# Performance work log

Hardware: AMD Instinct MI355X
Metric: run time of the kernel (lower is better)

## Reference

```python
import jax, jax.numpy as jnp
import numpy as np

BINS = 5
POINTS = 2
EPS_DIV = 1e-6
GN_GROUPS = 32
GN_EPS = 1e-5


def bilinear_sum(img, ys, xs):
    """Sum of bilinear samples with zero padding outside the image.
    img: (B, C, H, W); ys, xs: (B, K, H, W) absolute sample coords.
    Returns (B, C, H, W) = sum over K of bilinear(img, ys_k, xs_k)."""
    B, C, H, W = img.shape
    K = ys.shape[1]
    y0 = jnp.floor(ys)
    x0 = jnp.floor(xs)
    imgf = img.reshape(B, C, H * W)
    acc = jnp.zeros((B, C, K, H, W), img.dtype)
    for dy, dx in ((0, 0), (0, 1), (1, 0), (1, 1)):
        yi = y0 + dy
        xi = x0 + dx
        w = (1.0 - jnp.abs(ys - yi)) * (1.0 - jnp.abs(xs - xi))
        valid = (yi >= 0) & (yi <= H - 1) & (xi >= 0) & (xi <= W - 1)
        yc = jnp.clip(yi, 0, H - 1).astype(jnp.int32)
        xc = jnp.clip(xi, 0, W - 1).astype(jnp.int32)
        idx = (yc * W + xc).reshape(B, 1, K * H * W)
        g = jnp.take_along_axis(imgf, idx, axis=2).reshape(B, C, K, H, W)
        acc = acc + (w * valid.astype(img.dtype))[:, None] * g
    return acc.sum(axis=2)


def setup_inputs():
    key = jax.random.key(0)
    ks = jax.random.split(key, 6)
    B, C, H, W = 2, 256, 100, 152
    P, K = POINTS, BINS
    x = jax.random.normal(ks[0], (B, C, H, W), jnp.float32)
    offsets = jax.random.normal(ks[1], (B, P * K * 2, H, W), jnp.float32) * 2.0
    ef_w = jax.random.normal(ks[2], (P * C, C), jnp.float32) * 0.02
    ef_b = jnp.zeros((P * C,), jnp.float32)
    hm1_w = jax.random.normal(ks[3], (P, C, C), jnp.float32) * 0.02
    hm1_b = jnp.zeros((P, C), jnp.float32)
    hm2_w = jax.random.normal(ks[4], (P, C), jnp.float32) * 0.02
    hm2_b = jnp.zeros((P,), jnp.float32)
    merge_w = jax.random.normal(ks[5], (C, P * C), jnp.float32) * 0.02
    merge_b = jnp.zeros((C,), jnp.float32)
    gn_g = jnp.ones((C,), jnp.float32)
    gn_b = jnp.zeros((C,), jnp.float32)
    return {"x": x, "offsets": offsets, "ef_w": ef_w, "ef_b": ef_b,
            "hm1_w": hm1_w, "hm1_b": hm1_b, "hm2_w": hm2_w, "hm2_b": hm2_b,
            "merge_w": merge_w, "merge_b": merge_b, "gn_g": gn_g, "gn_b": gn_b}


def reference(x, offsets, ef_w, ef_b, hm1_w, hm1_b, hm2_w, hm2_b, merge_w, merge_b, gn_g, gn_b):
    B, C, H, W = x.shape
    P, K = POINTS, BINS
    # expand_feat: 1x1 conv C -> P*C
    ef = jnp.einsum('bchw,dc->bdhw', x, ef_w) + ef_b[None, :, None, None]
    efp = ef.reshape(B, P, C, H, W)
    # heatmap: grouped 1x1 conv (per-point) -> ReLU -> grouped 1x1 conv -> exp
    h = jax.nn.relu(jnp.einsum('bpchw,pdc->bpdhw', efp, hm1_w) + hm1_b[None, :, :, None, None])
    heat = jnp.exp(jnp.einsum('bpdhw,pd->bphw', h, hm2_w) + hm2_b[None, :, None, None])  # (B,P,H,W)
    # offsets: (B, P, K, 2, H, W) with channel layout [y, x] per bin.
    # base_offset cancels the [1,bins] kernel grid, so the deform conv with
    # all-ones weights is simply: sum over bins of bilinear samples at
    # (h + off_y, w + off_x).
    off = offsets.reshape(B, P, K, 2, H, W)
    hg = jnp.arange(H, dtype=x.dtype)[None, None, None, :, None]
    wg = jnp.arange(W, dtype=x.dtype)[None, None, None, None, :]
    ys = hg + off[:, :, :, 0]  # (B,P,K,H,W)
    xs = wg + off[:, :, :, 1]
    outs = []
    for p in range(P):
        # sample feat*heat (C channels) and heat (1 channel) together
        img = jnp.concatenate([efp[:, p] * heat[:, p][:, None], heat[:, p][:, None]], axis=1)
        s = bilinear_sum(img, ys[:, p], xs[:, p])  # (B, C+1, H, W)
        outs.append(s[:, :C] / (s[:, C:] + EPS_DIV))
    outs = jnp.concatenate(outs, axis=1)  # (B, P*C, H, W)
    merged = jnp.einsum('bchw,dc->bdhw', outs, merge_w) + merge_b[None, :, None, None]
    # GroupNorm(32, C) + ReLU
    g = merged.reshape(B, GN_GROUPS, C // GN_GROUPS, H, W)
    mu = g.mean(axis=(2, 3, 4), keepdims=True)
    var = g.var(axis=(2, 3, 4), keepdims=True)
    gn = ((g - mu) / jnp.sqrt(var + GN_EPS)).reshape(B, C, H, W)
    gn = gn * gn_g[None, :, None, None] + gn_b[None, :, None, None]
    return jax.nn.relu(gn)
```

## Files before the change

kernel.cpp:

```cpp
#include <hip/hip_runtime.h>

#define BINS 5
#define PTS  2
constexpr int Bx = 2, Cc = 256, Hh = 100, Ww = 152;
constexpr int HW = Hh * Ww;
constexpr int NTILE = 238;
constexpr float EPS_DIV = 1e-6f;
constexpr float GN_EPS  = 1e-5f;

typedef __attribute__((ext_vector_type(8))) _Float16 hfrag;
typedef __attribute__((ext_vector_type(2))) _Float16 h2;
typedef __attribute__((ext_vector_type(4))) float f32x4;

__device__ __forceinline__ ushort f2h(float f) {
    return __builtin_bit_cast(ushort, (_Float16)f);
}
__device__ __forceinline__ float hlo(unsigned u) {
    return (float)__builtin_bit_cast(_Float16, (ushort)(u & 0xffffu));
}
__device__ __forceinline__ float hhi(unsigned u) {
    return (float)__builtin_bit_cast(_Float16, (ushort)(u >> 16));
}

__global__ __launch_bounds__(256)
void k_wconv(const float* __restrict__ efw, const float* __restrict__ w1,
             const float* __restrict__ mw, ushort* __restrict__ wb)
{
    int gid = blockIdx.x * 256 + threadIdx.x;
    int e = gid * 4;
    int arr = e >> 17, off = e & 131071;
    const float* src = arr == 0 ? efw : (arr == 1 ? w1 : mw);
    float4 v = *(const float4*)(src + off);
    ushort4 o = { f2h(v.x), f2h(v.y), f2h(v.z), f2h(v.w) };
    *(ushort4*)(wb + e) = o;
}

__global__ __launch_bounds__(256)
void k_xt(const float* __restrict__ x, ushort* __restrict__ xbt)
{
    __shared__ float tile[32][33];
    const int t = threadIdx.x;
    const int hw0 = blockIdx.x * 32;
    const int c0 = blockIdx.y * 32;
    const int b = blockIdx.z;
    const float* xb = x + ((size_t)b * Cc + c0) * HW + hw0;
    const int tx = t & 31, ty = t >> 5;
    #pragma unroll
    for (int r = 0; r < 4; r++) {
        int c = ty + r * 8;
        tile[c][tx] = xb[(size_t)c * HW + tx];
    }
    __syncthreads();
    const int hwl = t >> 3, c4 = (t & 7) * 4;
    ushort4 o = { f2h(tile[c4 + 0][hwl]), f2h(tile[c4 + 1][hwl]),
                  f2h(tile[c4 + 2][hwl]), f2h(tile[c4 + 3][hwl]) };
    *(ushort4*)&xbt[((size_t)b * HW + hw0 + hwl) * Cc + c0 + c4] = o;
}

__global__ __launch_bounds__(256)
void k_ef(const ushort* __restrict__ xbt, const ushort* __restrict__ wbe,
          const float* __restrict__ efb, ushort* __restrict__ efp)
{
    __shared__ ushort As[128 * 72];
    __shared__ ushort Bs[64 * 72];
    const int t = threadIdx.x;
    const int wv = t >> 6, ln = t & 63;
    const int quad = ln >> 4, l16 = ln & 15;
    const int pix0 = blockIdx.x * 64;
    const int n0 = blockIdx.y * 128;
    const int b = blockIdx.z;
    const ushort* xb = xbt + (size_t)b * HW * Cc;

    f32x4 acc[2][4];
    #pragma unroll
    for (int i = 0; i < 2; i++)
        #pragma unroll
        for (int j = 0; j < 4; j++) acc[i][j] = (f32x4){0.f, 0.f, 0.f, 0.f};

    const int arow = t >> 3, acol = (t & 7) * 8;
    const int srow = t >> 3, scol = (t & 7) * 8;

    for (int k0 = 0; k0 < 256; k0 += 64) {
        #pragma unroll
        for (int r = 0; r < 4; r++) {
            int row = arow + r * 32;
            *(uint4*)&As[row * 72 + acol] =
                *(const uint4*)&wbe[(size_t)(n0 + row) * 256 + k0 + acol];
        }
        #pragma unroll
        for (int r = 0; r < 2; r++) {
            int row = srow + r * 32;
            int pq = pix0 + row; if (pq > HW - 1) pq = HW - 1;
            *(uint4*)&Bs[row * 72 + scol] =
                *(const uint4*)&xb[(size_t)pq * Cc + k0 + scol];
        }
        __syncthreads();
        #pragma unroll
        for (int kk = 0; kk < 64; kk += 32) {
            hfrag af[2], bfr[4];
            #pragma unroll
            for (int dt = 0; dt < 2; dt++)
                af[dt] = *(const hfrag*)&As[(wv * 32 + dt * 16 + l16) * 72 + kk + quad * 8];
            #pragma unroll
            for (int pt = 0; pt < 4; pt++)
                bfr[pt] = *(const hfrag*)&Bs[(pt * 16 + l16) * 72 + kk + quad * 8];
            #pragma unroll
            for (int dt = 0; dt < 2; dt++)
                #pragma unroll
                for (int pt = 0; pt < 4; pt++)
                    acc[dt][pt] = __builtin_amdgcn_mfma_f32_16x16x32_f16(
                        af[dt], bfr[pt], acc[dt][pt], 0, 0, 0);
        }
        __syncthreads();
    }

    float bias[2][4];
    #pragma unroll
    for (int dt = 0; dt < 2; dt++)
        #pragma unroll
        for (int r = 0; r < 4; r++)
            bias[dt][r] = efb[n0 + wv * 32 + dt * 16 + quad * 4 + r];
    #pragma unroll
    for (int dt = 0; dt < 2; dt++)
        #pragma unroll
        for (int pt = 0; pt < 4; pt++) {
            int pix = pt * 16 + l16;
            int ch = wv * 32 + dt * 16 + quad * 4;
            ushort4 o = { f2h(acc[dt][pt][0] + bias[dt][0]),
                          f2h(acc[dt][pt][1] + bias[dt][1]),
                          f2h(acc[dt][pt][2] + bias[dt][2]),
                          f2h(acc[dt][pt][3] + bias[dt][3]) };
            *(ushort4*)&As[pix * 136 + ch] = o;
        }
    __syncthreads();
    const int p = n0 >> 8, cbase = n0 & 255;
    ushort* outb = efp + (size_t)((b * PTS + p) * HW) * Cc;
    #pragma unroll
    for (int r = 0; r < 4; r++) {
        int pix = (t >> 4) + r * 16;
        int ch8 = (t & 15) * 8;
        if (pix0 + pix < HW)
            *(uint4*)&outb[(size_t)(pix0 + pix) * Cc + cbase + ch8] =
                *(const uint4*)&As[pix * 136 + ch8];
    }
}

__global__ __launch_bounds__(256)
void k_heat(const ushort* __restrict__ efp, const ushort* __restrict__ wb1,
            const float* __restrict__ b1, const float* __restrict__ w2,
            const float* __restrict__ b2, float* __restrict__ heat)
{
    __shared__ ushort As[256 * 72];
    __shared__ ushort Bs[64 * 72];
    __shared__ float red[4][64];
    const int t = threadIdx.x;
    const int wv = t >> 6, ln = t & 63;
    const int quad = ln >> 4, l16 = ln & 15;
    const int pix0 = blockIdx.x * 64;
    const int p = blockIdx.y;
    const int b = blockIdx.z;
    const ushort* efb_ = efp + (size_t)((b * PTS + p) * HW) * Cc;
    const ushort* w1p = wb1 + (size_t)p * Cc * Cc;

    f32x4 acc[4][4];
    #pragma unroll
    for (int i = 0; i < 4; i++)
        #pragma unroll
        for (int j = 0; j < 4; j++) acc[i][j] = (f32x4){0.f, 0.f, 0.f, 0.f};

    const int srow = t >> 3, scol = (t & 7) * 8;

    for (int k0 = 0; k0 < 256; k0 += 64) {
        #pragma unroll
        for (int r = 0; r < 8; r++) {
            int row = srow + r * 32;
            *(uint4*)&As[row * 72 + scol] =
                *(const uint4*)&w1p[(size_t)row * 256 + k0 + scol];
        }
        #pragma unroll
        for (int r = 0; r < 2; r++) {
            int row = srow + r * 32;
            int pq = pix0 + row; if (pq > HW - 1) pq = HW - 1;
            *(uint4*)&Bs[row * 72 + scol] =
                *(const uint4*)&efb_[(size_t)pq * Cc + k0 + scol];
        }
        __syncthreads();
        #pragma unroll
        for (int kk = 0; kk < 64; kk += 32) {
            hfrag af[4], bfr[4];
            #pragma unroll
            for (int dt = 0; dt < 4; dt++)
                af[dt] = *(const hfrag*)&As[(wv * 64 + dt * 16 + l16) * 72 + kk + quad * 8];
            #pragma unroll
            for (int pt = 0; pt < 4; pt++)
                bfr[pt] = *(const hfrag*)&Bs[(pt * 16 + l16) * 72 + kk + quad * 8];
            #pragma unroll
            for (int dt = 0; dt < 4; dt++)
                #pragma unroll
                for (int pt = 0; pt < 4; pt++)
                    acc[dt][pt] = __builtin_amdgcn_mfma_f32_16x16x32_f16(
                        af[dt], bfr[pt], acc[dt][pt], 0, 0, 0);
        }
        __syncthreads();
    }

    const float* b1p = b1 + p * 256;
    const float* w2p = w2 + p * 256;
    float s[4] = {0.f, 0.f, 0.f, 0.f};
    #pragma unroll
    for (int dt = 0; dt < 4; dt++) {
        int chb = wv * 64 + dt * 16 + quad * 4;
        float bb[4], ww[4];
        #pragma unroll
        for (int r = 0; r < 4; r++) { bb[r] = b1p[chb + r]; ww[r] = w2p[chb + r]; }
        #pragma unroll
        for (int pt = 0; pt < 4; pt++)
            #pragma unroll
            for (int r = 0; r < 4; r++) {
                float h = acc[dt][pt][r] + bb[r];
                h = h > 0.f ? h : 0.f;
                s[pt] += ww[r] * h;
            }
    }
    #pragma unroll
    for (int pt = 0; pt < 4; pt++) {
        s[pt] += __shfl_xor(s[pt], 16);
        s[pt] += __shfl_xor(s[pt], 32);
    }
    if (ln < 16) {
        #pragma unroll
        for (int pt = 0; pt < 4; pt++) red[wv][pt * 16 + ln] = s[pt];
    }
    __syncthreads();
    if (t < 64) {
        float v = red[0][t] + red[1][t] + red[2][t] + red[3][t] + b2[p];
        int m = pix0 + t;
        if (m < HW) heat[(size_t)(b * PTS + p) * HW + m] = expf(v);
    }
}

__global__ __launch_bounds__(256)
void k_sample(const ushort* __restrict__ efp, const float* __restrict__ heat,
              const float* __restrict__ offs, ushort* __restrict__ outs)
{
    __shared__ uint2 s_wo[32][20];
    const int t = threadIdx.x;
    const int bid = blockIdx.x;
    const int nx = (bid & 7) * 60 + (bid >> 3);
    if (nx >= 475) return;
    const int m0 = nx * 32;
    const int p = blockIdx.y;
    const int b = blockIdx.z;
    const float* heat_bp = heat + (size_t)(b * PTS + p) * HW;

    if (t < 32 * BINS) {
        int j = t / BINS, k = t % BINS;
        int hw = m0 + j;
        int hh = hw / Ww, ww = hw % Ww;
        int chy = (p * BINS + k) * 2;
        float oy = offs[((size_t)b * (PTS * BINS * 2) + chy)     * HW + hw];
        float ox = offs[((size_t)b * (PTS * BINS * 2) + chy + 1) * HW + hw];
        float ysf = (float)hh + oy;
        float xsf = (float)ww + ox;
        float y0 = floorf(ysf), x0 = floorf(xsf);
        #pragma unroll
        for (int dy = 0; dy < 2; dy++)
            #pragma unroll
            for (int dx = 0; dx < 2; dx++) {
                float yi = y0 + dy, xi = x0 + dx;
                float wgt = (1.f - fabsf(ysf - yi)) * (1.f - fabsf(xsf - xi));
                bool valid = (yi >= 0.f) && (yi <= (float)(Hh - 1)) &&
                             (xi >= 0.f) && (xi <= (float)(Ww - 1));
                int yc = (int)yi; yc = yc < 0 ? 0 : (yc > Hh - 1 ? Hh - 1 : yc);
                int xc = (int)xi; xc = xc < 0 ? 0 : (xc > Ww - 1 ? Ww - 1 : xc);
                int idx = yc * Ww + xc;
                float wh = valid ? wgt * heat_bp[idx] : 0.f;
                s_wo[j][k * 4 + dy * 2 + dx] =
                    make_uint2(__float_as_uint(wh), (unsigned)idx << 9);
            }
    }
    __syncthreads();
    if (t < 32) {
        float s = 0.f;
        #pragma unroll
        for (int u = 0; u < 20; u++) s += __uint_as_float(s_wo[t][u].x);
        float inv = 1.f / (s + EPS_DIV);
        #pragma unroll
        for (int u = 0; u < 20; u++) {
            float w = __uint_as_float(s_wo[t][u].x) * inv;
            unsigned hw16 = (unsigned)f2h(w);
            s_wo[t][u].x = hw16 | (hw16 << 16);
        }
    }
    __syncthreads();

    const int wv = t >> 6, ln = t & 63;
    const int half = ln >> 5, c8 = ln & 31;
    const char* efbase = (const char*)(efp + (size_t)((b * PTS + p) * HW) * Cc)
                         + c8 * 16;
    ushort* ob = outs + ((size_t)(b * HW + m0)) * (PTS * Cc) + p * Cc + c8 * 8;
    #pragma unroll
    for (int i = 0; i < 8; i += 2) {
        const int j = wv * 8 + i + half;
        h2 a0 = (h2){0, 0}, a1 = (h2){0, 0}, a2 = (h2){0, 0}, a3 = (h2){0, 0};
        #pragma unroll
        for (int u = 0; u < 20; u++) {
            uint2 wo = s_wo[j][u];
            uint4 v = *(const uint4*)(efbase + wo.y);
            h2 wp = __builtin_bit_cast(h2, wo.x);
            a0 += wp * __builtin_bit_cast(h2, v.x);
            a1 += wp * __builtin_bit_cast(h2, v.y);
            a2 += wp * __builtin_bit_cast(h2, v.z);
            a3 += wp * __builtin_bit_cast(h2, v.w);
        }
        uint4 o = { __builtin_bit_cast(unsigned, a0), __builtin_bit_cast(unsigned, a1),
                    __builtin_bit_cast(unsigned, a2), __builtin_bit_cast(unsigned, a3) };
        *(uint4*)(ob + (size_t)j * (PTS * Cc)) = o;
    }
}

__global__ __launch_bounds__(256)
void k_merge(const ushort* __restrict__ outs, const ushort* __restrict__ wbm,
             const float* __restrict__ mb, ushort* __restrict__ mgb,
             float* __restrict__ part2)
{
    __shared__ ushort As[64 * 72];
    __shared__ ushort Bs[64 * 72];
    const int t = threadIdx.x;
    const int wv = t >> 6, ln = t & 63;
    const int quad = ln >> 4, l16 = ln & 15;
    const int pix0 = blockIdx.x * 64;
    const int n0 = blockIdx.y * 64;
    const int b = blockIdx.z;
    const ushort* ob = outs + (size_t)b * HW * (PTS * Cc);

    f32x4 acc[4];
    #pragma unroll
    for (int j = 0; j < 4; j++) acc[j] = (f32x4){0.f, 0.f, 0.f, 0.f};

    const int srow = t >> 3, scol = (t & 7) * 8;

    for (int k0 = 0; k0 < 512; k0 += 64) {
        #pragma unroll
        for (int r = 0; r < 2; r++) {
            int row = srow + r * 32;
            *(uint4*)&As[row * 72 + scol] =
                *(const uint4*)&wbm[(size_t)(n0 + row) * 512 + k0 + scol];
        }
        #pragma unroll
        for (int r = 0; r < 2; r++) {
            int row = srow + r * 32;
            int pq = pix0 + row; if (pq > HW - 1) pq = HW - 1;
            *(uint4*)&Bs[row * 72 + scol] =
                *(const uint4*)&ob[(size_t)pq * (PTS * Cc) + k0 + scol];
        }
        __syncthreads();
        #pragma unroll
        for (int kk = 0; kk < 64; kk += 32) {
            hfrag af = *(const hfrag*)&As[(wv * 16 + l16) * 72 + kk + quad * 8];
            #pragma unroll
            for (int pt = 0; pt < 4; pt++) {
                hfrag bfr = *(const hfrag*)&Bs[(pt * 16 + l16) * 72 + kk + quad * 8];
                acc[pt] = __builtin_amdgcn_mfma_f32_16x16x32_f16(
                    af, bfr, acc[pt], 0, 0, 0);
            }
        }
        __syncthreads();
    }

    const int ch = n0 + wv * 16 + quad * 4;
    float bias[4];
    #pragma unroll
    for (int r = 0; r < 4; r++) bias[r] = mb[ch + r];

    float sacc = 0.f, qacc = 0.f;
    #pragma unroll
    for (int pt = 0; pt < 4; pt++) {
        int pix = pix0 + pt * 16 + l16;
        if (pix < HW) {
            #pragma unroll
            for (int r = 0; r < 4; r++) {
                float v = acc[pt][r] + bias[r];
                mgb[((size_t)b * Cc + ch + r) * HW + pix] = f2h(v);
                sacc += v; qacc += v * v;
            }
        }
    }
    #pragma unroll
    for (int off = 1; off <= 16; off <<= 1) {
        sacc += __shfl_xor(sacc, off);
        qacc += __shfl_xor(qacc, off);
    }
    if ((ln & 31) == 0) {
        int g = (n0 >> 3) + wv * 2 + (quad >> 1);
        size_t idx = ((size_t)(b * 32 + g) * NTILE + blockIdx.x) * 2;
        part2[idx + 0] = sacc;
        part2[idx + 1] = qacc;
    }
}

__global__ __launch_bounds__(256)
void k_gnfinal(const float* __restrict__ part2, float* __restrict__ statf)
{
    const int bg = blockIdx.x;
    const int t = threadIdx.x;
    float s = 0.f, q = 0.f;
    if (t < NTILE) {
        s = part2[((size_t)bg * NTILE + t) * 2 + 0];
        q = part2[((size_t)bg * NTILE + t) * 2 + 1];
    }
    #pragma unroll
    for (int off = 1; off <= 32; off <<= 1) {
        s += __shfl_xor(s, off);
        q += __shfl_xor(q, off);
    }
    __shared__ float rs[4], rq[4];
    int wid = t >> 6;
    if ((t & 63) == 0) { rs[wid] = s; rq[wid] = q; }
    __syncthreads();
    if (t == 0) {
        float S = rs[0] + rs[1] + rs[2] + rs[3];
        float Q = rq[0] + rq[1] + rq[2] + rq[3];
        const float n = 8.f * HW;
        float mean = S / n;
        float var  = Q / n - mean * mean;
        statf[bg * 2 + 0] = mean;
        statf[bg * 2 + 1] = rsqrtf(var + GN_EPS);
    }
}

__global__ __launch_bounds__(256)
void k_gnapply(const ushort* __restrict__ mgb, const float* __restrict__ statf,
               const float* __restrict__ gg, const float* __restrict__ gb,
               float* __restrict__ out)
{
    const int i8 = blockIdx.x * 256 + threadIdx.x;
    const int i = i8 * 8;
    const int CHW = Cc * HW;
    const int b = i / CHW;
    const int r = i - b * CHW;
    const int c = r / HW;
    const int g = c >> 3;
    float mean = statf[(b * 32 + g) * 2 + 0];
    float istd = statf[(b * 32 + g) * 2 + 1];
    float sc = istd * gg[c];
    float sh = gb[c] - mean * sc;
    uint4 v = *(const uint4*)(mgb + i);
    float4 o0, o1;
    o0.x = fmaxf(hlo(v.x) * sc + sh, 0.f);
    o0.y = fmaxf(hhi(v.x) * sc + sh, 0.f);
    o0.z = fmaxf(hlo(v.y) * sc + sh, 0.f);
    o0.w = fmaxf(hhi(v.y) * sc + sh, 0.f);
    o1.x = fmaxf(hlo(v.z) * sc + sh, 0.f);
    o1.y = fmaxf(hhi(v.z) * sc + sh, 0.f);
    o1.z = fmaxf(hlo(v.w) * sc + sh, 0.f);
    o1.w = fmaxf(hhi(v.w) * sc + sh, 0.f);
    *(float4*)(out + i)     = o0;
    *(float4*)(out + i + 4) = o1;
}

extern "C" void kernel_launch(void* const* d_in, const int* in_sizes, int n_in,
                              void* d_out, int out_size, void* d_ws, size_t ws_size,
                              hipStream_t stream)
{
    const float* x    = (const float*)d_in[0];
    const float* offs = (const float*)d_in[1];
    const float* efw  = (const float*)d_in[2];
    const float* efb  = (const float*)d_in[3];
    const float* w1   = (const float*)d_in[4];
    const float* b1   = (const float*)d_in[5];
    const float* w2   = (const float*)d_in[6];
    const float* b2   = (const float*)d_in[7];
    const float* mw   = (const float*)d_in[8];
    const float* mb   = (const float*)d_in[9];
    const float* gg   = (const float*)d_in[10];
    const float* gb   = (const float*)d_in[11];
    float* out = (float*)d_out;

    ushort* wb    = (ushort*)d_ws;
    ushort* wbe   = wb;
    ushort* wb1   = wb + 131072;
    ushort* wbm   = wb + 262144;
    ushort* efp   = wb + 393216;
    ushort* outsb = efp + (size_t)Bx * PTS * HW * Cc;
    ushort* xbt   = outsb + (size_t)Bx * HW * PTS * Cc;
    ushort* mgb   = xbt + (size_t)Bx * HW * Cc;
    float*  heat  = (float*)(mgb + (size_t)Bx * Cc * HW);
    float*  part2 = heat + (size_t)Bx * PTS * HW;
    float*  statf = part2 + (size_t)64 * NTILE * 2;

    dim3 blk(256);
    k_wconv  <<<dim3(384),              blk, 0, stream>>>(efw, w1, mw, wb);
    k_xt     <<<dim3(475, 8, Bx),       blk, 0, stream>>>(x, xbt);
    k_ef     <<<dim3(238, 4, Bx),       blk, 0, stream>>>(xbt, wbe, efb, efp);
    k_heat   <<<dim3(238, PTS, Bx),     blk, 0, stream>>>(efp, wb1, b1, w2, b2, heat);
    k_sample <<<dim3(480, PTS, Bx),     blk, 0, stream>>>(efp, heat, offs, outsb);
    k_merge  <<<dim3(NTILE, 4, Bx),     blk, 0, stream>>>(outsb, wbm, mb, mgb, part2);
    k_gnfinal<<<dim3(64),               blk, 0, stream>>>(part2, statf);
    k_gnapply<<<dim3(Bx * Cc * HW / 8 / 256), blk, 0, stream>>>(mgb, statf, gg, gb, out);
}
```

Measured before the change: 208.0 us.

## Make expand and heat GEMMs persistent with resident weights and async LDS double-buffering

The expand-feature and heatmap 1x1-conv GEMMs become persistent 512-thread blocks. Each block loads its full 128x256 weight slice into LDS once with direct global-to-LDS loads, then loops over pixel tiles using double-buffered, XOR-swizzled B tiles with vmcnt-based waits. This is meant to stop reloading weights for every tile and to hide global-load latency. Heat is split across two channel halves that write partial sums, and a new small kernel adds them with the bias and applies exp. The cost is one extra launch, much larger LDS per block, and fewer blocks (240 per kernel) to keep the GPU busy.

```diff
diff --git a/kernel.cpp b/kernel.cpp
--- a/kernel.cpp
+++ b/kernel.cpp
@@ -22,6 +22,10 @@
     return (float)__builtin_bit_cast(_Float16, (ushort)(u >> 16));
 }
 
+#define GLL16(g, l) __builtin_amdgcn_global_load_lds( \
+    (const __attribute__((address_space(1))) unsigned*)(g), \
+    (__attribute__((address_space(3))) unsigned*)(l), 16, 0, 0)
+
 __global__ __launch_bounds__(256)
 void k_wconv(const float* __restrict__ efw, const float* __restrict__ w1,
              const float* __restrict__ mw, ushort* __restrict__ wb)
@@ -57,186 +61,254 @@
     *(ushort4*)&xbt[((size_t)b * HW + hw0 + hwl) * Cc + c0 + c4] = o;
 }
 
-__global__ __launch_bounds__(256)
+__global__ __launch_bounds__(512)
 void k_ef(const ushort* __restrict__ xbt, const ushort* __restrict__ wbe,
           const float* __restrict__ efb, ushort* __restrict__ efp)
 {
-    __shared__ ushort As[128 * 72];
-    __shared__ ushort Bs[64 * 72];
-    const int t = threadIdx.x;
+    __shared__ ushort Alds[128 * 256];
+    __shared__ ushort Bl0[64 * 256];
+    __shared__ ushort Bl1[64 * 256];
+    const int t  = threadIdx.x;
     const int wv = t >> 6, ln = t & 63;
     const int quad = ln >> 4, l16 = ln & 15;
-    const int pix0 = blockIdx.x * 64;
-    const int n0 = blockIdx.y * 128;
-    const int b = blockIdx.z;
+    const int mwv = wv & 3, ngr = wv >> 2;
+    const int xr = l16 & 7;
+    const int bx = blockIdx.x;
+    const int n0 = blockIdx.y;
+    const int b  = blockIdx.z;
     const ushort* xb = xbt + (size_t)b * HW * Cc;
-
-    f32x4 acc[2][4];
-    #pragma unroll
-    for (int i = 0; i < 2; i++)
-        #pragma unroll
-        for (int j = 0; j < 4; j++) acc[i][j] = (f32x4){0.f, 0.f, 0.f, 0.f};
-
-    const int arow = t >> 3, acol = (t & 7) * 8;
-    const int srow = t >> 3, scol = (t & 7) * 8;
-
-    for (int k0 = 0; k0 < 256; k0 += 64) {
-        #pragma unroll
-        for (int r = 0; r < 4; r++) {
-            int row = arow + r * 32;
-            *(uint4*)&As[row * 72 + acol] =
-                *(const uint4*)&wbe[(size_t)(n0 + row) * 256 + k0 + acol];
-        }
-        #pragma unroll
-        for (int r = 0; r < 2; r++) {
-            int row = srow + r * 32;
-            int pq = pix0 + row; if (pq > HW - 1) pq = HW - 1;
-            *(uint4*)&Bs[row * 72 + scol] =
-                *(const uint4*)&xb[(size_t)pq * Cc + k0 + scol];
-        }
-        __syncthreads();
-        #pragma unroll
-        for (int kk = 0; kk < 64; kk += 32) {
-            hfrag af[2], bfr[4];
-            #pragma unroll
-            for (int dt = 0; dt < 2; dt++)
-                af[dt] = *(const hfrag*)&As[(wv * 32 + dt * 16 + l16) * 72 + kk + quad * 8];
-            #pragma unroll
-            for (int pt = 0; pt < 4; pt++)
-                bfr[pt] = *(const hfrag*)&Bs[(pt * 16 + l16) * 72 + kk + quad * 8];
-            #pragma unroll
-            for (int dt = 0; dt < 2; dt++)
-                #pragma unroll
-                for (int pt = 0; pt < 4; pt++)
-                    acc[dt][pt] = __builtin_amdgcn_mfma_f32_16x16x32_f16(
-                        af[dt], bfr[pt], acc[dt][pt], 0, 0, 0);
-        }
-        __syncthreads();
-    }
+    const ushort* wA = wbe + (size_t)n0 * 128 * 256;
+    const int ntl = (237 - bx) / 30 + 1;
+
+    #pragma unroll
+    for (int j = 0; j < 8; j++) {
+        int unit = j * 512 + t;
+        int row = unit >> 5, c8 = unit & 31;
+        const ushort* g = wA + row * 256 + ((c8 ^ (row & 7)) << 3);
+        ushort* l = Alds + (j * 512 + wv * 64) * 8;
+        GLL16(g, l);
+    }
+    auto stageB = [&](int tt, ushort* dst) {
+        int tp0 = tt * 64;
+        #pragma unroll
+        for (int j = 0; j < 4; j++) {
+            int unit = j * 512 + t;
+            int prow = unit >> 5, c8 = unit & 31;
+            int pq = tp0 + prow; if (pq > HW - 1) pq = HW - 1;
+            const ushort* g = xb + (size_t)pq * 256 + ((c8 ^ (prow & 7)) << 3);
+            ushort* l = dst + (j * 512 + wv * 64) * 8;
+            GLL16(g, l);
+        }
+    };
+    stageB(bx, Bl0);
+    stageB(bx + 30, Bl1);
+    asm volatile("s_waitcnt vmcnt(4)" ::: "memory");
+    __builtin_amdgcn_s_barrier();
+    __builtin_amdgcn_sched_barrier(0);
 
     float bias[2][4];
     #pragma unroll
     for (int dt = 0; dt < 2; dt++)
         #pragma unroll
         for (int r = 0; r < 4; r++)
-            bias[dt][r] = efb[n0 + wv * 32 + dt * 16 + quad * 4 + r];
-    #pragma unroll
-    for (int dt = 0; dt < 2; dt++)
-        #pragma unroll
-        for (int pt = 0; pt < 4; pt++) {
-            int pix = pt * 16 + l16;
-            int ch = wv * 32 + dt * 16 + quad * 4;
-            ushort4 o = { f2h(acc[dt][pt][0] + bias[dt][0]),
-                          f2h(acc[dt][pt][1] + bias[dt][1]),
-                          f2h(acc[dt][pt][2] + bias[dt][2]),
-                          f2h(acc[dt][pt][3] + bias[dt][3]) };
-            *(ushort4*)&As[pix * 136 + ch] = o;
-        }
-    __syncthreads();
-    const int p = n0 >> 8, cbase = n0 & 255;
-    ushort* outb = efp + (size_t)((b * PTS + p) * HW) * Cc;
-    #pragma unroll
-    for (int r = 0; r < 4; r++) {
-        int pix = (t >> 4) + r * 16;
-        int ch8 = (t & 15) * 8;
-        if (pix0 + pix < HW)
-            *(uint4*)&outb[(size_t)(pix0 + pix) * Cc + cbase + ch8] =
-                *(const uint4*)&As[pix * 136 + ch8];
-    }
-}
-
-__global__ __launch_bounds__(256)
+            bias[dt][r] = efb[n0 * 128 + mwv * 32 + dt * 16 + quad * 4 + r];
+
+    const int aof0 = (mwv * 32 + l16) * 256;
+    const int aof1 = (mwv * 32 + 16 + l16) * 256;
+    const int bof0 = (ngr * 32 + l16) * 256;
+    const int bof1 = (ngr * 32 + 16 + l16) * 256;
+    const int p_ = n0 >> 1;
+    const int cb = (n0 & 1) * 128 + mwv * 32;
+    ushort* outb = efp + (size_t)((b * PTS + p_) * HW) * Cc;
+
+    for (int it = 0; it < ntl; it++) {
+        const int tp0 = (bx + it * 30) * 64;
+        const ushort* bb = (it & 1) ? Bl1 : Bl0;
+        f32x4 acc[2][2];
+        #pragma unroll
+        for (int i = 0; i < 2; i++)
+            #pragma unroll
+            for (int j = 0; j < 2; j++) acc[i][j] = (f32x4){0.f, 0.f, 0.f, 0.f};
+        #pragma unroll
+        for (int s = 0; s < 8; s++) {
+            const int co = (((s * 4 + quad) ^ xr) << 3);
+            hfrag a0 = *(const hfrag*)&Alds[aof0 + co];
+            hfrag a1 = *(const hfrag*)&Alds[aof1 + co];
+            hfrag b0 = *(const hfrag*)&bb[bof0 + co];
+            hfrag b1 = *(const hfrag*)&bb[bof1 + co];
+            acc[0][0] = __builtin_amdgcn_mfma_f32_16x16x32_f16(a0, b0, acc[0][0], 0, 0, 0);
+            acc[0][1] = __builtin_amdgcn_mfma_f32_16x16x32_f16(a0, b1, acc[0][1], 0, 0, 0);
+            acc[1][0] = __builtin_amdgcn_mfma_f32_16x16x32_f16(a1, b0, acc[1][0], 0, 0, 0);
+            acc[1][1] = __builtin_amdgcn_mfma_f32_16x16x32_f16(a1, b1, acc[1][1], 0, 0, 0);
+        }
+        #pragma unroll
+        for (int dt = 0; dt < 2; dt++)
+            #pragma unroll
+            for (int pt = 0; pt < 2; pt++) {
+                int pix = tp0 + ngr * 32 + pt * 16 + l16;
+                if (pix < HW) {
+                    ushort4 o = { f2h(acc[dt][pt][0] + bias[dt][0]),
+                                  f2h(acc[dt][pt][1] + bias[dt][1]),
+                                  f2h(acc[dt][pt][2] + bias[dt][2]),
+                                  f2h(acc[dt][pt][3] + bias[dt][3]) };
+                    *(ushort4*)&outb[(size_t)pix * Cc + cb + dt * 16 + quad * 4] = o;
+                }
+            }
+        if (it + 1 < ntl) {
+            __builtin_amdgcn_s_barrier();
+            if (it + 2 < ntl) {
+                stageB(bx + (it + 2) * 30, (it & 1) ? Bl1 : Bl0);
+                asm volatile("s_waitcnt vmcnt(4)" ::: "memory");
+            } else {
+                asm volatile("s_waitcnt vmcnt(0)" ::: "memory");
+            }
+            __builtin_amdgcn_s_barrier();
+            __builtin_amdgcn_sched_barrier(0);
+        }
+    }
+}
+
+__global__ __launch_bounds__(512)
 void k_heat(const ushort* __restrict__ efp, const ushort* __restrict__ wb1,
             const float* __restrict__ b1, const float* __restrict__ w2,
-            const float* __restrict__ b2, float* __restrict__ heat)
-{
-    __shared__ ushort As[256 * 72];
-    __shared__ ushort Bs[64 * 72];
-    __shared__ float red[4][64];
-    const int t = threadIdx.x;
+            float* __restrict__ hp)
+{
+    __shared__ ushort Alds[128 * 256];
+    __shared__ ushort Bl0[64 * 256];
+    __shared__ ushort Bl1[64 * 256];
+    __shared__ float red[2][4][32];
+    const int t  = threadIdx.x;
     const int wv = t >> 6, ln = t & 63;
     const int quad = ln >> 4, l16 = ln & 15;
-    const int pix0 = blockIdx.x * 64;
-    const int p = blockIdx.y;
-    const int b = blockIdx.z;
-    const ushort* efb_ = efp + (size_t)((b * PTS + p) * HW) * Cc;
-    const ushort* w1p = wb1 + (size_t)p * Cc * Cc;
-
-    f32x4 acc[4][4];
-    #pragma unroll
-    for (int i = 0; i < 4; i++)
-        #pragma unroll
-        for (int j = 0; j < 4; j++) acc[i][j] = (f32x4){0.f, 0.f, 0.f, 0.f};
-
-    const int srow = t >> 3, scol = (t & 7) * 8;
-
-    for (int k0 = 0; k0 < 256; k0 += 64) {
-        #pragma unroll
-        for (int r = 0; r < 8; r++) {
-            int row = srow + r * 32;
-            *(uint4*)&As[row * 72 + scol] =
-                *(const uint4*)&w1p[(size_t)row * 256 + k0 + scol];
-        }
-        #pragma unroll
-        for (int r = 0; r < 2; r++) {
-            int row = srow + r * 32;
-            int pq = pix0 + row; if (pq > HW - 1) pq = HW - 1;
-            *(uint4*)&Bs[row * 72 + scol] =
-                *(const uint4*)&efb_[(size_t)pq * Cc + k0 + scol];
-        }
-        __syncthreads();
-        #pragma unroll
-        for (int kk = 0; kk < 64; kk += 32) {
-            hfrag af[4], bfr[4];
-            #pragma unroll
-            for (int dt = 0; dt < 4; dt++)
-                af[dt] = *(const hfrag*)&As[(wv * 64 + dt * 16 + l16) * 72 + kk + quad * 8];
-            #pragma unroll
-            for (int pt = 0; pt < 4; pt++)
-                bfr[pt] = *(const hfrag*)&Bs[(pt * 16 + l16) * 72 + kk + quad * 8];
-            #pragma unroll
-            for (int dt = 0; dt < 4; dt++)
-                #pragma unroll
-                for (int pt = 0; pt < 4; pt++)
-                    acc[dt][pt] = __builtin_amdgcn_mfma_f32_16x16x32_f16(
-                        af[dt], bfr[pt], acc[dt][pt], 0, 0, 0);
-        }
-        __syncthreads();
-    }
+    const int mwv = wv & 3, ngr = wv >> 2;
+    const int xr = l16 & 7;
+    const int bx = blockIdx.x;
+    const int p  = blockIdx.y >> 1;
+    const int n0 = blockIdx.y & 1;
+    const int b  = blockIdx.z;
+    const ushort* eb = efp + (size_t)((b * PTS + p) * HW) * Cc;
+    const ushort* wA = wb1 + (size_t)p * Cc * Cc + (size_t)n0 * 128 * 256;
+    const int ntl = (237 - bx) / 30 + 1;
+
+    #pragma unroll
+    for (int j = 0; j < 8; j++) {
+        int unit = j * 512 + t;
+        int row = unit >> 5, c8 = unit & 31;
+        const ushort* g = wA + row * 256 + ((c8 ^ (row & 7)) << 3);
+        ushort* l = Alds + (j * 512 + wv * 64) * 8;
+        GLL16(g, l);
+    }
+    auto stageB = [&](int tt, ushort* dst) {
+        int tp0 = tt * 64;
+        #pragma unroll
+        for (int j = 0; j < 4; j++) {
+            int unit = j * 512 + t;
+            int prow = unit >> 5, c8 = unit & 31;
+            int pq = tp0 + prow; if (pq > HW - 1) pq = HW - 1;
+            const ushort* g = eb + (size_t)pq * 256 + ((c8 ^ (prow & 7)) << 3);
+            ushort* l = dst + (j * 512 + wv * 64) * 8;
+            GLL16(g, l);
+        }
+    };
+    stageB(bx, Bl0);
+    stageB(bx + 30, Bl1);
+    asm volatile("s_waitcnt vmcnt(4)" ::: "memory");
+    __builtin_amdgcn_s_barrier();
+    __builtin_amdgcn_sched_barrier(0);
 
     const float* b1p = b1 + p * 256;
     const float* w2p = w2 + p * 256;
-    float s[4] = {0.f, 0.f, 0.f, 0.f};
-    #pragma unroll
-    for (int dt = 0; dt < 4; dt++) {
-        int chb = wv * 64 + dt * 16 + quad * 4;
-        float bb[4], ww[4];
-        #pragma unroll
-        for (int r = 0; r < 4; r++) { bb[r] = b1p[chb + r]; ww[r] = w2p[chb + r]; }
-        #pragma unroll
-        for (int pt = 0; pt < 4; pt++)
+    float b1v[2][4], w2v[2][4];
+    #pragma unroll
+    for (int dt = 0; dt < 2; dt++)
+        #pragma unroll
+        for (int r = 0; r < 4; r++) {
+            int gch = n0 * 128 + mwv * 32 + dt * 16 + quad * 4 + r;
+            b1v[dt][r] = b1p[gch];
+            w2v[dt][r] = w2p[gch];
+        }
+
+    const int aof0 = (mwv * 32 + l16) * 256;
+    const int aof1 = (mwv * 32 + 16 + l16) * 256;
+    const int bof0 = (ngr * 32 + l16) * 256;
+    const int bof1 = (ngr * 32 + 16 + l16) * 256;
+    float* hpo = hp + (size_t)n0 * (Bx * PTS * HW) + (size_t)(b * PTS + p) * HW;
+
+    for (int it = 0; it < ntl; it++) {
+        const int tp0 = (bx + it * 30) * 64;
+        const ushort* bb = (it & 1) ? Bl1 : Bl0;
+        f32x4 acc[2][2];
+        #pragma unroll
+        for (int i = 0; i < 2; i++)
+            #pragma unroll
+            for (int j = 0; j < 2; j++) acc[i][j] = (f32x4){0.f, 0.f, 0.f, 0.f};
+        #pragma unroll
+        for (int s = 0; s < 8; s++) {
+            const int co = (((s * 4 + quad) ^ xr) << 3);
+            hfrag a0 = *(const hfrag*)&Alds[aof0 + co];
+            hfrag a1 = *(const hfrag*)&Alds[aof1 + co];
+            hfrag b0 = *(const hfrag*)&bb[bof0 + co];
+            hfrag b1f = *(const hfrag*)&bb[bof1 + co];
+            acc[0][0] = __builtin_amdgcn_mfma_f32_16x16x32_f16(a0, b0, acc[0][0], 0, 0, 0);
+            acc[0][1] = __builtin_amdgcn_mfma_f32_16x16x32_f16(a0, b1f, acc[0][1], 0, 0, 0);
+            acc[1][0] = __builtin_amdgcn_mfma_f32_16x16x32_f16(a1, b0, acc[1][0], 0, 0, 0);
+            acc[1][1] = __builtin_amdgcn_mfma_f32_16x16x32_f16(a1, b1f, acc[1][1], 0, 0, 0);
+        }
+        float s0 = 0.f, s1 = 0.f;
+        #pragma unroll
+        for (int dt = 0; dt < 2; dt++)
             #pragma unroll
             for (int r = 0; r < 4; r++) {
-                float h = acc[dt][pt][r] + bb[r];
-                h = h > 0.f ? h : 0.f;
-                s[pt] += ww[r] * h;
-            }
-    }
-    #pragma unroll
-    for (int pt = 0; pt < 4; pt++) {
-        s[pt] += __shfl_xor(s[pt], 16);
-        s[pt] += __shfl_xor(s[pt], 32);
-    }
-    if (ln < 16) {
-        #pragma unroll
-        for (int pt = 0; pt < 4; pt++) red[wv][pt * 16 + ln] = s[pt];
-    }
-    __syncthreads();
-    if (t < 64) {
-        float v = red[0][t] + red[1][t] + red[2][t] + red[3][t] + b2[p];
-        int m = pix0 + t;
-        if (m < HW) heat[(size_t)(b * PTS + p) * HW + m] = expf(v);
-    }
+                float h0 = acc[dt][0][r] + b1v[dt][r];
+                float h1 = acc[dt][1][r] + b1v[dt][r];
+                h0 = h0 > 0.f ? h0 : 0.f;
+                h1 = h1 > 0.f ? h1 : 0.f;
+                s0 += w2v[dt][r] * h0;
+                s1 += w2v[dt][r] * h1;
+            }
+        s0 += __shfl_xor(s0, 16); s0 += __shfl_xor(s0, 32);
+        s1 += __shfl_xor(s1, 16); s1 += __shfl_xor(s1, 32);
+        if (ln < 16) {
+            red[ngr][mwv][ln]      = s0;
+            red[ngr][mwv][16 + ln] = s1;
+        }
+        asm volatile("s_waitcnt lgkmcnt(0)" ::: "memory");
+        __builtin_amdgcn_s_barrier();
+        if (t < 64) {
+            int g = t >> 5, i32 = t & 31;
+            float v = red[g][0][i32] + red[g][1][i32] + red[g][2][i32] + red[g][3][i32];
+            int pix = tp0 + t;
+            if (pix < HW) hpo[pix] = v;
+        }
+        if (it + 1 < ntl) {
+            if (it + 2 < ntl) {
+                stageB(bx + (it + 2) * 30, (it & 1) ? Bl1 : Bl0);
+                asm volatile("s_waitcnt vmcnt(4)" ::: "memory");
+            } else {
+                asm volatile("s_waitcnt vmcnt(0)" ::: "memory");
+            }
+            __builtin_amdgcn_s_barrier();
+            __builtin_amdgcn_sched_barrier(0);
+        }
+    }
+}
+
+__global__ __launch_bounds__(256)
+void k_hexp(const float* __restrict__ hp, const float* __restrict__ b2,
+            float* __restrict__ heat)
+{
+    int t4 = blockIdx.x * 256 + threadIdx.x;
+    if (t4 >= (Bx * PTS * HW) / 4) return;
+    int i = t4 * 4;
+    float b2v = b2[(i / HW) & 1];
+    float4 a = *(const float4*)(hp + i);
+    float4 c = *(const float4*)(hp + (size_t)(Bx * PTS * HW) + i);
+    float4 o;
+    o.x = expf(a.x + c.x + b2v);
+    o.y = expf(a.y + c.y + b2v);
+    o.z = expf(a.z + c.z + b2v);
+    o.w = expf(a.w + c.w + b2v);
+    *(float4*)(heat + i) = o;
 }
 
 __global__ __launch_bounds__(256)
@@ -488,12 +560,14 @@
     float*  heat  = (float*)(mgb + (size_t)Bx * Cc * HW);
     float*  part2 = heat + (size_t)Bx * PTS * HW;
     float*  statf = part2 + (size_t)64 * NTILE * 2;
+    float*  hp    = statf + 128;
 
     dim3 blk(256);
     k_wconv  <<<dim3(384),              blk, 0, stream>>>(efw, w1, mw, wb);
     k_xt     <<<dim3(475, 8, Bx),       blk, 0, stream>>>(x, xbt);
-    k_ef     <<<dim3(238, 4, Bx),       blk, 0, stream>>>(xbt, wbe, efb, efp);
-    k_heat   <<<dim3(238, PTS, Bx),     blk, 0, stream>>>(efp, wb1, b1, w2, b2, heat);
+    k_ef     <<<dim3(30, 4, Bx),  dim3(512), 0, stream>>>(xbt, wbe, efb, efp);
+    k_heat   <<<dim3(30, 4, Bx),  dim3(512), 0, stream>>>(efp, wb1, b1, w2, hp);
+    k_hexp   <<<dim3(60),               blk, 0, stream>>>(hp, b2, heat);
     k_sample <<<dim3(480, PTS, Bx),     blk, 0, stream>>>(efp, heat, offs, outsb);
     k_merge  <<<dim3(NTILE, 4, Bx),     blk, 0, stream>>>(outsb, wbm, mb, mgb, part2);
     k_gnfinal<<<dim3(64),               blk, 0, stream>>>(part2, statf);
```

Measured after the change: 209.3 us. About the same (+0.7%).
